# Optimization experiments

Hardware: AMD Instinct MI355X
Metric: run time of the kernel (lower is better)

The kernel has to match this reference:

```python
import jax, jax.numpy as jnp
import numpy as np

H = 12  # max_heads

def setup_inputs() -> dict:
    key = jax.random.key(0)
    ks = jax.random.split(key, 5)
    B, N, E = 8, 1024, 768
    return {
        "x": jax.random.normal(ks[0], (B, N, E), dtype=jnp.float32),
        "w_qkv": jax.random.normal(ks[1], (3 * E, E), dtype=jnp.float32) * 0.02,
        "b_qkv": jax.random.normal(ks[2], (3 * E,), dtype=jnp.float32) * 0.02,
        "w_proj": jax.random.normal(ks[3], (E, E), dtype=jnp.float32) * 0.02,
        "b_proj": jax.random.normal(ks[4], (E,), dtype=jnp.float32) * 0.02,
        "active_heads": 8,
    }

def reference(x, w_qkv, b_qkv, w_proj, b_proj, active_heads):
    B, N, E = x.shape
    D = E // H
    scale = D ** -0.5
    # qkv projection: [B,N,3E] -> [3,B,H,N,D]
    qkv = (x @ w_qkv.T + b_qkv).reshape(B, N, 3, H, D)
    qkv = jnp.transpose(qkv, (2, 0, 3, 1, 4))
    q, k, v = qkv[0], qkv[1], qkv[2]
    # head mask from active_heads (static int)
    head_mask = (jnp.arange(H) < active_heads).astype(x.dtype)
    m = head_mask[None, :, None, None]
    q = q * m
    k = k * m
    v = v * m
    attn = jax.nn.softmax(jnp.einsum("bhqd,bhkd->bhqk", q, k) * scale, axis=-1)
    out = jnp.einsum("bhqk,bhkd->bhqd", attn, v)
    out = jnp.transpose(out, (0, 2, 1, 3)).reshape(B, N, E)
    channel_mask = jnp.repeat(head_mask, D)  # [E]
    out = out * channel_mask[None, None, :]
    return out @ w_proj.T + b_proj
```

## Files before the change

kernel.cpp:

```cpp
#include <hip/hip_runtime.h>
#include <hip/hip_fp16.h>

#define NH 12
#define BSZ 8
#define NSEQ 1024
#define EDIM 768
#define DH 64

typedef _Float16 f16;
typedef f16 half8 __attribute__((ext_vector_type(8)));
typedef f16 half4 __attribute__((ext_vector_type(4)));
typedef float f32x4 __attribute__((ext_vector_type(4)));
typedef unsigned int u32;
typedef u32 u32x2 __attribute__((ext_vector_type(2)));

static __device__ __forceinline__ void gload16(const void* g, void* l) {
    __builtin_amdgcn_global_load_lds((const __attribute__((address_space(1))) u32*)g,
                                     (__attribute__((address_space(3))) u32*)l, 16, 0, 0);
}
static __device__ __forceinline__ u32 pkrtz(float a, float b) {
    auto h = __builtin_amdgcn_cvt_pkrtz(a, b);
    return __builtin_bit_cast(u32, h);
}
#define MFMA16(a, b, c) __builtin_amdgcn_mfma_f32_16x16x32_f16((a), (b), (c), 0, 0, 0)

__global__ void cvt_all_kernel(const float* __restrict__ x, const float* __restrict__ wq,
                               const float* __restrict__ wp, f16* __restrict__ dst) {
    const int NX = BSZ * NSEQ * EDIM;
    const int NWQ = 3 * EDIM * EDIM;
    int i = (blockIdx.x * blockDim.x + threadIdx.x) * 4;
    const float* s;
    int j;
    if (i < NX) { s = x; j = i; }
    else if (i < NX + NWQ) { s = wq; j = i - NX; }
    else { s = wp; j = i - NX - NWQ; }
    float4 v = *(const float4*)(s + j);
    half4 o = { (f16)v.x, (f16)v.y, (f16)v.z, (f16)v.w };
    *(half4*)(dst + i) = o;
}

template<int MODE>
__global__ __launch_bounds__(256) void gemm_kernel(
    const f16* __restrict__ A, const f16* __restrict__ Wt, const float* __restrict__ bias,
    f16* __restrict__ qbuf, f16* __restrict__ kbuf, f16* __restrict__ vbuf,
    float* __restrict__ outp, const int* __restrict__ activep, int K, int NC)
{
    __shared__ __align__(16) f16 Ah[2][2][2][4][64][8];
    __shared__ __align__(16) f16 Bh[2][2][2][4][64][8];

    constexpr int NB = (MODE == 0) ? 18 : 6;
    const int lin = blockIdx.x;
    const int xcd = lin & 7, pos = lin >> 3;
    const int bx = pos % NB;
    const int my = xcd + (pos / NB) * 8;
    const int c0 = bx * 128;
    const int m0 = my * 128;
    if (MODE == 0) {
        int hb = (c0 % EDIM) >> 6;
        if (hb >= *activep) return;
    }
    const int tid = threadIdx.x;
    const int lane = tid & 63;
    const int wid  = tid >> 6;
    const int wr = wid >> 1, wc = wid & 1;
    const int r16 = lane & 15, rg = lane >> 4;

    f32x4 acc[4][4];
#pragma unroll
    for (int i = 0; i < 4; ++i)
#pragma unroll
        for (int j = 0; j < 4; ++j)
            acc[i][j] = f32x4{0.f, 0.f, 0.f, 0.f};

    const int sA = wid >> 1, kA = wid & 1;
    const int sB = wid & 1,  kB = wid >> 1;
    const f16* gA = A  + (size_t)(m0 + sA * 64 + r16) * K + kA * 32 + rg * 8;
    const f16* gB = Wt + (size_t)(c0 + sB * 64 + r16) * K + kB * 32 + rg * 8;
    const int nkt = K / 64;

    auto stage = [&](int buf, int kt) {
#pragma unroll
        for (int f = 0; f < 4; ++f) {
            gload16(gA + (size_t)(f * 16) * K + kt * 64, &Ah[buf][sA][kA][f][0][0]);
            gload16(gB + (size_t)(f * 16) * K + kt * 64, &Bh[buf][sB][kB][f][0][0]);
        }
    };

    stage(0, 0);
    __syncthreads();
    int cur = 0;
    for (int kt = 0; kt < nkt; ++kt) {
        if (kt + 1 < nkt) stage(cur ^ 1, kt + 1);
        half8 af[2][4], bf[2][4];
#pragma unroll
        for (int kk = 0; kk < 2; ++kk)
#pragma unroll
            for (int f = 0; f < 4; ++f) {
                af[kk][f] = *(const half8*)&Ah[cur][wr][kk][f][lane][0];
                bf[kk][f] = *(const half8*)&Bh[cur][wc][kk][f][lane][0];
            }
#pragma unroll
        for (int fm = 0; fm < 4; ++fm)
#pragma unroll
            for (int fn = 0; fn < 4; ++fn) {
                acc[fm][fn] = MFMA16(af[0][fm], bf[0][fn], acc[fm][fn]);
                acc[fm][fn] = MFMA16(af[1][fm], bf[1][fn], acc[fm][fn]);
            }
        __syncthreads();
        cur ^= 1;
    }

#pragma unroll
    for (int fn = 0; fn < 4; ++fn) {
        const int c = c0 + wc * 64 + fn * 16 + r16;
        const float bv = bias[c];
#pragma unroll
        for (int fm = 0; fm < 4; ++fm) {
            const int mbase = m0 + wr * 64 + fm * 16 + rg * 4;
#pragma unroll
            for (int r = 0; r < 4; ++r) {
                const float val = acc[fm][fn][r] + bv;
                const int m = mbase + r;
                if (MODE == 1) {
                    outp[(size_t)m * EDIM + c] = val;
                } else {
                    const int s  = c / EDIM;
                    const int cc = c % EDIM;
                    const int hh = cc >> 6, d = cc & 63;
                    const int bb = m >> 10, n = m & 1023;
                    f16* dst = (s == 0) ? qbuf : ((s == 1) ? kbuf : vbuf);
                    dst[(((size_t)bb * NH + hh) * NSEQ + n) * DH + d] = (f16)val;
                }
            }
        }
    }
}

__global__ __launch_bounds__(256) void vtrans_kernel(const f16* __restrict__ vbuf,
                                                     f16* __restrict__ vtb,
                                                     const int* __restrict__ activep) {
    const int b = blockIdx.z, h = blockIdx.y;
    if (h >= *activep) return;
    const int n0 = blockIdx.x * 64;
    __shared__ __align__(16) f16 T[64][72];
    const f16* src = vbuf + (((size_t)b * NH + h) * NSEQ + n0) * DH;
    f16* dst = vtb + ((size_t)b * NH + h) * DH * NSEQ;
    const int t = threadIdx.x;
    const int rn = t >> 2, rc = t & 3;
    *(half8*)&T[rn][rc * 16]     = *(const half8*)&src[(size_t)rn * DH + rc * 16];
    *(half8*)&T[rn][rc * 16 + 8] = *(const half8*)&src[(size_t)rn * DH + rc * 16 + 8];
    __syncthreads();
    const int d = t >> 2, nc = (t & 3) * 16;
    half8 o0, o1;
#pragma unroll
    for (int j = 0; j < 8; ++j) {
        o0[j] = T[nc + j][d];
        o1[j] = T[nc + 8 + j][d];
    }
    *(half8*)&dst[(size_t)d * NSEQ + n0 + nc]     = o0;
    *(half8*)&dst[(size_t)d * NSEQ + n0 + nc + 8] = o1;
}

__global__ __launch_bounds__(256) void attn_kernel(
    const f16* __restrict__ qbuf, const f16* __restrict__ kbuf, const f16* __restrict__ vtb,
    f16* __restrict__ ctx, const int* __restrict__ activep)
{
    __shared__ __align__(16) f16 Kh[2][64][64];
    __shared__ __align__(16) f16 Vh[2][64][64];
    __shared__ __align__(16) f16 Ph[4][16][64];

    const int b = blockIdx.z, h = blockIdx.y;
    const int q0 = blockIdx.x * 64;
    const int tid = threadIdx.x, lane = tid & 63, wid = tid >> 6;

    if (h >= *activep) {
        const int r = tid >> 2, cp = tid & 3;
        half8 z = { (f16)0,(f16)0,(f16)0,(f16)0,(f16)0,(f16)0,(f16)0,(f16)0 };
        size_t base = ((size_t)b * NSEQ + q0 + r) * EDIM + h * DH + cp * 16;
        *(half8*)&ctx[base]     = z;
        *(half8*)&ctx[base + 8] = z;
        return;
    }

    const size_t hb = (((size_t)b * NH + h) * NSEQ) * DH;
    const f16* Q  = qbuf + hb;
    const char* Kp = (const char*)(kbuf + hb);
    const char* Vp = (const char*)(vtb + hb);

    const int ql = lane & 15;
    const int g  = lane >> 4;
    const int q7 = ql & 7;

    half8 qb0, qb1;
    {
        const f16* qp = Q + (size_t)(q0 + wid * 16 + ql) * DH + g * 8;
        qb0 = *(const half8*)qp        * (f16)0.125f;
        qb1 = *(const half8*)(qp + 32) * (f16)0.125f;
    }

    const int srow8 = lane >> 3;
    const int schk  = (lane & 7) ^ srow8;

    auto stage = [&](int buf, int kt) {
        const char* kb = Kp + (size_t)kt * 8192;
#pragma unroll
        for (int i = 0; i < 2; ++i) {
            const int r = wid * 16 + i * 8 + srow8;
            gload16(kb + (size_t)r * 128 + schk * 16, &Kh[buf][wid * 16 + i * 8][0]);
            gload16(Vp + (size_t)r * (NSEQ * 2) + (size_t)kt * 128 + schk * 16,
                    &Vh[buf][wid * 16 + i * 8][0]);
        }
    };

    f32x4 oacc[4];
#pragma unroll
    for (int i = 0; i < 4; ++i) oacc[i] = f32x4{0.f, 0.f, 0.f, 0.f};
    float mr = -INFINITY, lr = 0.f;

    char* prow = (char*)&Ph[wid][ql][0];

    stage(0, 0);
    const int NT = NSEQ / 64;
    for (int kt = 0; kt < NT; ++kt) {
        const int cur = kt & 1;
        __syncthreads();
        if (kt + 1 < NT) stage(cur ^ 1, kt + 1);

        f32x4 st[4];
        __builtin_amdgcn_s_setprio(1);
#pragma unroll
        for (int s = 0; s < 4; ++s) {
            f32x4 t = f32x4{0.f, 0.f, 0.f, 0.f};
            t = MFMA16(*(const half8*)((const char*)&Kh[cur][16 * s + ql][0] + ((g ^ q7) << 4)),       qb0, t);
            t = MFMA16(*(const half8*)((const char*)&Kh[cur][16 * s + ql][0] + (((4 | g) ^ q7) << 4)), qb1, t);
            st[s] = t;
        }
        __builtin_amdgcn_s_setprio(0);

        float pmax;
        {
            float m0v = fmaxf(fmaxf(st[0][0], st[0][1]), fmaxf(st[0][2], st[0][3]));
            float m1v = fmaxf(fmaxf(st[1][0], st[1][1]), fmaxf(st[1][2], st[1][3]));
            float m2v = fmaxf(fmaxf(st[2][0], st[2][1]), fmaxf(st[2][2], st[2][3]));
            float m3v = fmaxf(fmaxf(st[3][0], st[3][1]), fmaxf(st[3][2], st[3][3]));
            pmax = fmaxf(fmaxf(m0v, m1v), fmaxf(m2v, m3v));
        }
        pmax = fmaxf(pmax, __shfl_xor(pmax, 16));
        pmax = fmaxf(pmax, __shfl_xor(pmax, 32));
        const float mnew = fmaxf(mr, pmax);
        const float sc = __expf(mr - mnew);
        float psum = 0.f;
#pragma unroll
        for (int s = 0; s < 4; ++s)
#pragma unroll
            for (int r = 0; r < 4; ++r) {
                float p = __expf(st[s][r] - mnew);
                st[s][r] = p;
                psum += p;
            }
        psum += __shfl_xor(psum, 16);
        psum += __shfl_xor(psum, 32);
        lr = lr * sc + psum;
        mr = mnew;

#pragma unroll
        for (int r = 0; r < 4; ++r) {
            const float scr = __shfl(sc, (g << 2) | r);
            oacc[0][r] *= scr; oacc[1][r] *= scr; oacc[2][r] *= scr; oacc[3][r] *= scr;
        }

#pragma unroll
        for (int s = 0; s < 4; ++s) {
            u32x2 w = { pkrtz(st[s][0], st[s][1]), pkrtz(st[s][2], st[s][3]) };
            *(u32x2*)(prow + ((32 * s + 8 * g) ^ (q7 << 4))) = w;
        }
        const half8 pa0 = *(const half8*)(prow + ((16 * g) ^ (q7 << 4)));
        const half8 pa1 = *(const half8*)(prow + ((64 + 16 * g) ^ (q7 << 4)));

        __builtin_amdgcn_s_setprio(1);
#pragma unroll
        for (int db = 0; db < 4; ++db) {
            oacc[db] = MFMA16(pa0, *(const half8*)((const char*)&Vh[cur][16 * db + ql][0] + ((g ^ q7) << 4)),       oacc[db]);
            oacc[db] = MFMA16(pa1, *(const half8*)((const char*)&Vh[cur][16 * db + ql][0] + (((4 | g) ^ q7) << 4)), oacc[db]);
        }
        __builtin_amdgcn_s_setprio(0);
    }

#pragma unroll
    for (int r = 0; r < 4; ++r) {
        const float li = 1.0f / __shfl(lr, (g << 2) | r);
        const int n = q0 + wid * 16 + (g << 2) + r;
#pragma unroll
        for (int db = 0; db < 4; ++db)
            ctx[((size_t)b * NSEQ + n) * EDIM + h * DH + db * 16 + ql] = (f16)(oacc[db][r] * li);
    }
}

extern "C" void kernel_launch(void* const* d_in, const int* in_sizes, int n_in,
                              void* d_out, int out_size, void* d_ws, size_t ws_size,
                              hipStream_t stream) {
    const float* x      = (const float*)d_in[0];
    const float* w_qkv  = (const float*)d_in[1];
    const float* b_qkv  = (const float*)d_in[2];
    const float* w_proj = (const float*)d_in[3];
    const float* b_proj = (const float*)d_in[4];
    const int*   active = (const int*)d_in[5];
    float* out = (float*)d_out;

    char* ws = (char*)d_ws;
    const size_t n_x  = (size_t)BSZ * NSEQ * EDIM;
    const size_t n_wq = (size_t)3 * EDIM * EDIM;
    const size_t n_wp = (size_t)EDIM * EDIM;
    const size_t n_hd = (size_t)BSZ * NH * NSEQ * DH;

    f16* xh   = (f16*)ws;
    f16* wqh  = xh + n_x;
    f16* wph  = wqh + n_wq;
    f16* qh   = wph + n_wp;
    f16* kh   = qh + n_hd;
    f16* vh   = kh + n_hd;
    f16* ctxh = vh + n_hd;
    f16* vtb  = xh;

    const size_t n_cvt = n_x + n_wq + n_wp;
    cvt_all_kernel<<<(int)(n_cvt / 4 / 256), 256, 0, stream>>>(x, w_qkv, w_proj, xh);

    gemm_kernel<0><<<dim3(18 * 64), 256, 0, stream>>>(
        xh, wqh, b_qkv, qh, kh, vh, nullptr, active, EDIM, 3 * EDIM);

    vtrans_kernel<<<dim3(NSEQ / 64, NH, BSZ), 256, 0, stream>>>(vh, vtb, active);

    attn_kernel<<<dim3(NSEQ / 64, NH, BSZ), 256, 0, stream>>>(qh, kh, vtb, ctxh, active);

    gemm_kernel<1><<<dim3(6 * 64), 256, 0, stream>>>(
        ctxh, wph, b_proj, nullptr, nullptr, nullptr, out, active, EDIM, EDIM);
}
```

Measured before the change: 132.3 us.

## Load GEMM MFMA fragments directly from global memory, dropping LDS staging

Replaces the LDS double-buffered tiling in the GEMM kernel with direct per-wave global loads of MFMA fragments into registers, using a two-stage register ping-pong and a compile-time K. This removes the shared-memory traffic and the __syncthreads barriers. In exchange, the four waves no longer share tiles, so global/L2 traffic goes up and each wave makes strided 16-byte loads. Register pressure also rises.

Measured after the change: 178.0 us. 1.35x slower.

```diff
diff --git a/kernel.cpp b/kernel.cpp
--- a/kernel.cpp
+++ b/kernel.cpp
@@ -43,12 +43,12 @@
 __global__ __launch_bounds__(256) void gemm_kernel(
     const f16* __restrict__ A, const f16* __restrict__ Wt, const float* __restrict__ bias,
     f16* __restrict__ qbuf, f16* __restrict__ kbuf, f16* __restrict__ vbuf,
-    float* __restrict__ outp, const int* __restrict__ activep, int K, int NC)
+    float* __restrict__ outp, const int* __restrict__ activep, int Kdummy, int NC)
 {
-    __shared__ __align__(16) f16 Ah[2][2][2][4][64][8];
-    __shared__ __align__(16) f16 Bh[2][2][2][4][64][8];
-
+    constexpr int K = EDIM;
+    constexpr int NKT = K / 32;
     constexpr int NB = (MODE == 0) ? 18 : 6;
+
     const int lin = blockIdx.x;
     const int xcd = lin & 7, pos = lin >> 3;
     const int bx = pos % NB;
@@ -72,43 +72,33 @@
         for (int j = 0; j < 4; ++j)
             acc[i][j] = f32x4{0.f, 0.f, 0.f, 0.f};
 
-    const int sA = wid >> 1, kA = wid & 1;
-    const int sB = wid & 1,  kB = wid >> 1;
-    const f16* gA = A  + (size_t)(m0 + sA * 64 + r16) * K + kA * 32 + rg * 8;
-    const f16* gB = Wt + (size_t)(c0 + sB * 64 + r16) * K + kB * 32 + rg * 8;
-    const int nkt = K / 64;
-
-    auto stage = [&](int buf, int kt) {
-#pragma unroll
-        for (int f = 0; f < 4; ++f) {
-            gload16(gA + (size_t)(f * 16) * K + kt * 64, &Ah[buf][sA][kA][f][0][0]);
-            gload16(gB + (size_t)(f * 16) * K + kt * 64, &Bh[buf][sB][kB][f][0][0]);
-        }
-    };
-
-    stage(0, 0);
-    __syncthreads();
-    int cur = 0;
-    for (int kt = 0; kt < nkt; ++kt) {
-        if (kt + 1 < nkt) stage(cur ^ 1, kt + 1);
-        half8 af[2][4], bf[2][4];
-#pragma unroll
-        for (int kk = 0; kk < 2; ++kk)
-#pragma unroll
-            for (int f = 0; f < 4; ++f) {
-                af[kk][f] = *(const half8*)&Ah[cur][wr][kk][f][lane][0];
-                bf[kk][f] = *(const half8*)&Bh[cur][wc][kk][f][lane][0];
-            }
-#pragma unroll
-        for (int fm = 0; fm < 4; ++fm)
-#pragma unroll
-            for (int fn = 0; fn < 4; ++fn) {
-                acc[fm][fn] = MFMA16(af[0][fm], bf[0][fn], acc[fm][fn]);
-                acc[fm][fn] = MFMA16(af[1][fm], bf[1][fn], acc[fm][fn]);
-            }
-        __syncthreads();
-        cur ^= 1;
-    }
+    const f16* gA = A  + (size_t)(m0 + wr * 64 + r16) * K + rg * 8;
+    const f16* gB = Wt + (size_t)(c0 + wc * 64 + r16) * K + rg * 8;
+
+#define LOADFRAGS(aa, bb, kk)                                             \
+    _Pragma("unroll")                                                     \
+    for (int f = 0; f < 4; ++f) {                                         \
+        aa[f] = *(const half8*)(gA + (size_t)(f * 16) * K + (kk) * 32);   \
+        bb[f] = *(const half8*)(gB + (size_t)(f * 16) * K + (kk) * 32);   \
+    }
+#define DOMFMA(aa, bb)                                                    \
+    _Pragma("unroll")                                                     \
+    for (int fm = 0; fm < 4; ++fm)                                        \
+        _Pragma("unroll")                                                 \
+        for (int fn = 0; fn < 4; ++fn)                                    \
+            acc[fm][fn] = MFMA16(aa[fm], bb[fn], acc[fm][fn]);
+
+    half8 aP[4], bP[4], aN[4], bN[4];
+    LOADFRAGS(aP, bP, 0)
+#pragma unroll 1
+    for (int kk = 0; kk + 2 <= NKT; kk += 2) {
+        LOADFRAGS(aN, bN, kk + 1)
+        DOMFMA(aP, bP)
+        if (kk + 2 < NKT) { LOADFRAGS(aP, bP, kk + 2) }
+        DOMFMA(aN, bN)
+    }
+#undef LOADFRAGS
+#undef DOMFMA
 
 #pragma unroll
     for (int fn = 0; fn < 4; ++fn) {
```
